# Kernel optimization log

Measured on AMD Instinct MI355X. Metric: run time of the kernel, lower is better.

Reference implementation:

```python
import jax, jax.numpy as jnp
import numpy as np

KSIZE = 3
SCALE = 2


def setup_inputs() -> dict:
    key = jax.random.key(0)
    k1, k2, k3, k4 = jax.random.split(key, 4)
    B, C, H, W = 8, 3, 512, 512
    h, w = H // SCALE, W // SCALE
    return {
        "images": jax.random.uniform(k1, (B, C, H, W), jnp.float32),
        "kernels": jax.random.uniform(k2, (B, KSIZE ** 2, h, w), jnp.float32),
        "offsets_x": jax.random.uniform(k3, (B, KSIZE ** 2, h, w), jnp.float32),
        "offsets_y": jax.random.uniform(k4, (B, KSIZE ** 2, h, w), jnp.float32),
    }


def _softround(x, alpha=1.0):
    two_pi = 2.0 * jnp.pi
    return x - alpha * (jnp.sin(two_pi * x) / two_pi)


def _batch_bli(im, x, y):
    # im: [B, H, W, 3] channel-last; x, y: [B, N] float coords
    B, N = x.shape
    x0 = jnp.floor(x).astype(jnp.int32)
    x1 = x0 + 1
    y0 = jnp.floor(y).astype(jnp.int32)
    y1 = y0 + 1
    # original clamps x by im.shape[2] and y by im.shape[1] (square images)
    x0 = jnp.clip(x0, 0, im.shape[2] - 1)
    x1 = jnp.clip(x1, 0, im.shape[2] - 1)
    y0 = jnp.clip(y0, 0, im.shape[1] - 1)
    y1 = jnp.clip(y1, 0, im.shape[1] - 1)
    bidx = jnp.arange(B)[:, None]
    # vectorized gather of the four corners; flatten like torch.cat of [3]-vectors
    Ia = im[bidx, x0, y0].reshape(-1)  # [B*N*3]
    Ib = im[bidx, x0, y1].reshape(-1)
    Ic = im[bidx, x1, y0].reshape(-1)
    Id = im[bidx, x1, y1].reshape(-1)
    scale_w = (1.0 / ((x1 - x0) * (y1 - y0))).reshape(-1)  # [B*N]
    # faithful to the original's (scrambling) reshape semantics
    m1 = jnp.concatenate([x1 - x, x - x0], axis=1).astype(jnp.float32)  # [B, 2N]
    m1 = jnp.tile(m1.reshape(B * N, 1, 1, 2), (1, 2, 1, 1))             # [BN,2,1,2]
    m2 = jnp.stack([Ib, Ia, Id, Ic], axis=1).reshape(B * N, 2, 2, 3)    # [BN,2,2,3]
    m3 = jnp.concatenate([y1 - y, y - y0], axis=1).astype(jnp.float32)
    m3 = m3.reshape(B * N, 1, 2, 1)                                     # [BN,1,2,1]
    t = jnp.matmul(m1, m2).transpose(0, 3, 2, 1)  # [BN,3,1,2]
    out = jnp.matmul(t, m3).reshape(B * N, 3)     # [BN,3]
    return scale_w[:, None] * out


def reference(images, kernels, offsets_x, offsets_y):
    B = images.shape[0]
    h, w = images.shape[2] // SCALE, images.shape[3] // SCALE
    kernels = kernels.transpose(0, 2, 3, 1)      # [B,h,w,9]
    ox = offsets_x.transpose(0, 2, 3, 1)         # [B,h,w,9]
    oy = offsets_y.transpose(0, 2, 3, 1)
    u = jnp.arange(h, dtype=jnp.float32) + 0.5 * SCALE - 0.5
    kx = jnp.repeat(jnp.arange(KSIZE), KSIZE).astype(jnp.float32)  # 0,0,0,1,1,1,2,2,2
    ky = jnp.tile(jnp.arange(KSIZE), KSIZE).astype(jnp.float32)    # 0,1,2,0,1,2,0,1,2
    # original broadcasts u.reshape(h,1) over the w axis (requires h == w)
    coords_x = ox + KSIZE / 2 + kx + u[:, None]
    coords_y = oy + KSIZE / 2 + ky + u[:, None]
    im = images.transpose(0, 2, 3, 1)  # [B,H,W,3]
    pix = _batch_bli(im, coords_x.reshape(B, -1), coords_y.reshape(B, -1))
    pix_hr = pix.reshape(B, h, w, KSIZE ** 2, 3)
    out = jnp.sum(kernels[..., None] * pix_hr, axis=-2)  # [B,h,w,3]
    return _softround(out * 255.0)
```

## Files before the change

kernel.cpp:

```cpp
#include <hip/hip_runtime.h>
#include <math.h>

#define BATCH 8
#define HI 512
#define WI 512
#define HO 256
#define WO 256
#define PLANE (HI*WI)
#define OPIX (HO*WO)
#define LROWS 68
#define LCOLS 10
#define LQ 11

__global__ __launch_bounds__(256) void downsampler_kernel(
    const float* __restrict__ images,
    const float* __restrict__ kernels,
    const float* __restrict__ offx,
    const float* __restrict__ offy,
    float* __restrict__ out)
{
    __shared__ float4 simg[LROWS * LQ];

    const int blk  = blockIdx.x;
    const int b    = blk >> 8;
    const int ihx  = (blk >> 2) & 63;
    const int w0   = (blk & 3) << 6;
    const int tid  = threadIdx.x;
    const int lane = tid & 63;
    const int iw   = w0 + lane;
    const int ih   = (ihx << 2) + (tid >> 6);

    const float* offxb = offx    + (size_t)b * 9 * OPIX;
    const float* offyb = offy    + (size_t)b * 9 * OPIX;
    const float* kernb = kernels + (size_t)b * 9 * OPIX;

    const int pl   = ih * WO + iw;
    const int pix2 = pl & (OPIX / 2 - 1);

    float  ox_[9], oy_[9], kv_[9];
    float2 sx_[9], sy_[9];
    #pragma unroll
    for (int k = 0; k < 9; ++k) {
        ox_[k] = offxb[k * OPIX + pl];
        oy_[k] = offyb[k * OPIX + pl];
        kv_[k] = kernb[k * OPIX + pl];
        sx_[k] = ((const float2*)(offxb + k * OPIX))[pix2];
        sy_[k] = ((const float2*)(offyb + k * OPIX))[pix2];
    }

    {
        const float* imb = images + (size_t)b * 3 * PLANE;
        #pragma unroll
        for (int ii = 0; ii < 3; ++ii) {
            const int i = tid + ii * 256;
            if (i < LROWS * LCOLS) {
                const int row = i / LCOLS;
                const int col = i - row * LCOLS;
                const int r = w0 + 2 + row;
                int c = r - 4 + col;
                c = c < 0 ? 0 : c;
                const float* src = imb + r * WI + c;
                simg[row * LQ + col] =
                    make_float4(src[0], src[PLANE], src[2 * PLANE], 0.0f);
            }
        }
    }
    __builtin_amdgcn_sched_barrier(0);
    __syncthreads();

    const bool flip = (ih < 128);
    const float uu_own = (float)iw + 0.5f;
    const float uu_s0  = (float)((2 * iw) & 255) + 0.5f;
    const float uu_s1  = uu_s0 + 1.0f;

    float acc0 = 0.f, acc1 = 0.f, acc2 = 0.f;

    #pragma unroll
    for (int k = 0; k < 9; ++k) {
        const float kxf = (float)(k / 3);
        const float kyf = (float)(k - 3 * (k / 3));
        const float cx = ((ox_[k] + 1.5f) + kxf) + uu_own;
        const float cy = ((oy_[k] + 1.5f) + kyf) + uu_own;
        const int x0 = (int)floorf(cx);
        const int y0 = (int)floorf(cy);
        const int rowrel = x0 - 2 - w0;
        const int colq   = y0 - x0 + 4;
        const float4* qa = &simg[rowrel * LQ + (colq - 1)];
        const float4 Ia = qa[1];
        const float4 Ib = qa[2];
        const float4 Ic = qa[LQ];
        const float4 Id = qa[LQ + 1];

        const int ta = 2 * k, tb = 2 * k + 1;
        const int sel_a = (ta >= 9) ? 1 : 0;
        const int sel_b = (tb >= 9) ? 1 : 0;
        const int ks_a = ta - 9 * sel_a;
        const int ks_b = tb - 9 * sel_b;
        const float uu_a = sel_a ? uu_s1 : uu_s0;
        const float uu_b = sel_b ? uu_s1 : uu_s0;
        const float oxa  = sel_a ? sx_[ks_a].y : sx_[ks_a].x;
        const float oya  = sel_a ? sy_[ks_a].y : sy_[ks_a].x;
        const float oxb2 = sel_b ? sx_[ks_b].y : sx_[ks_b].x;
        const float oyb2 = sel_b ? sy_[ks_b].y : sy_[ks_b].x;
        const float kxa = (float)(ks_a / 3), kya = (float)(ks_a - 3 * (ks_a / 3));
        const float kxb = (float)(ks_b / 3), kyb = (float)(ks_b - 3 * (ks_b / 3));

        const float cxa = ((oxa + 1.5f) + kxa) + uu_a;
        const float cya = ((oya + 1.5f) + kya) + uu_a;
        const float cxb = ((oxb2 + 1.5f) + kxb) + uu_b;
        const float cyb = ((oyb2 + 1.5f) + kyb) + uu_b;
        const float fxa = cxa - floorf(cxa);
        const float fya = cya - floorf(cya);
        const float fxb = cxb - floorf(cxb);
        const float fyb = cyb - floorf(cyb);
        const float w0w = flip ? (1.0f - fxa) : fxa;
        const float w1w = flip ? (1.0f - fxb) : fxb;
        const float v0w = flip ? (1.0f - fya) : fya;
        const float v1w = flip ? (1.0f - fyb) : fyb;

        const float w0v0 = w0w * v0w, w1v0 = w1w * v0w;
        const float w0v1 = w0w * v1w, w1v1 = w1w * v1w;

        const float p0 = w0v0 * Ib.x + w1v0 * Ic.x + w0v1 * Id.y + w1v1 * Ia.z;
        const float p1 = w0v0 * Ia.x + w1v0 * Ib.y + w0v1 * Ic.y + w1v1 * Id.z;
        const float p2 = w0v0 * Id.x + w1v0 * Ia.y + w0v1 * Ib.z + w1v1 * Ic.z;

        acc0 += kv_[k] * p0;
        acc1 += kv_[k] * p1;
        acc2 += kv_[k] * p2;
    }

    const float TWO_PI_INV = 0.15915494309189533577f;
    const size_t obase = ((size_t)b * OPIX + (size_t)pl) * 3;
    const float z0 = acc0 * 255.0f;
    const float z1 = acc1 * 255.0f;
    const float z2 = acc2 * 255.0f;
    const float r0s = z0 - rintf(z0);
    const float r1s = z1 - rintf(z1);
    const float r2s = z2 - rintf(z2);
    out[obase + 0] = z0 - __builtin_amdgcn_sinf(r0s) * TWO_PI_INV;
    out[obase + 1] = z1 - __builtin_amdgcn_sinf(r1s) * TWO_PI_INV;
    out[obase + 2] = z2 - __builtin_amdgcn_sinf(r2s) * TWO_PI_INV;
}

extern "C" void kernel_launch(void* const* d_in, const int* in_sizes, int n_in,
                              void* d_out, int out_size, void* d_ws, size_t ws_size,
                              hipStream_t stream) {
    const float* images  = (const float*)d_in[0];
    const float* kernels = (const float*)d_in[1];
    const float* offx    = (const float*)d_in[2];
    const float* offy    = (const float*)d_in[3];
    float* out = (float*)d_out;

    dim3 grid(BATCH * 64 * 4);
    dim3 block(256);
    hipLaunchKernelGGL(downsampler_kernel, grid, block, 0, stream,
                       images, kernels, offx, offy, out);
}
```

Measured before the change: 113.0 us.

## Process paired half-plane pixels per thread to share scrambled offset loads

Each thread now computes two output pixels, pl and pl+HALF. Because of the reference's reshape scrambling, both pixels use the same scrambled float2 offset pair for their weights, so those loads and the fractional-weight math are shared and the flip branch is removed. The grid is halved, launch bounds request 4 blocks, and the LDS byte offsets are computed before the barrier to overlap with the shared-memory fill. The cost is higher register pressure and fewer blocks in flight.

```diff
diff --git a/kernel.cpp b/kernel.cpp
--- a/kernel.cpp
+++ b/kernel.cpp
@@ -8,11 +8,12 @@
 #define WO 256
 #define PLANE (HI*WI)
 #define OPIX (HO*WO)
+#define HALF (OPIX/2)
 #define LROWS 68
 #define LCOLS 10
 #define LQ 11
 
-__global__ __launch_bounds__(256) void downsampler_kernel(
+__global__ __launch_bounds__(256, 4) void downsampler_kernel(
     const float* __restrict__ images,
     const float* __restrict__ kernels,
     const float* __restrict__ offx,
@@ -22,30 +23,37 @@
     __shared__ float4 simg[LROWS * LQ];
 
     const int blk  = blockIdx.x;
-    const int b    = blk >> 8;
-    const int ihx  = (blk >> 2) & 63;
+    const int b    = blk >> 7;
+    const int ihx  = (blk >> 2) & 31;
     const int w0   = (blk & 3) << 6;
     const int tid  = threadIdx.x;
     const int lane = tid & 63;
     const int iw   = w0 + lane;
-    const int ih   = (ihx << 2) + (tid >> 6);
+    const int ihA  = (ihx << 2) + (tid >> 6);
+    const int plA  = ihA * WO + iw;
+    const int plB  = plA + HALF;
 
     const float* offxb = offx    + (size_t)b * 9 * OPIX;
     const float* offyb = offy    + (size_t)b * 9 * OPIX;
     const float* kernb = kernels + (size_t)b * 9 * OPIX;
 
-    const int pl   = ih * WO + iw;
-    const int pix2 = pl & (OPIX / 2 - 1);
-
-    float  ox_[9], oy_[9], kv_[9];
+    float oxA[9], oyA[9], oxB[9], oyB[9];
+    #pragma unroll
+    for (int k = 0; k < 9; ++k) {
+        oxA[k] = offxb[k * OPIX + plA];
+        oyA[k] = offyb[k * OPIX + plA];
+        oxB[k] = offxb[k * OPIX + plB];
+        oyB[k] = offyb[k * OPIX + plB];
+    }
+
     float2 sx_[9], sy_[9];
-    #pragma unroll
-    for (int k = 0; k < 9; ++k) {
-        ox_[k] = offxb[k * OPIX + pl];
-        oy_[k] = offyb[k * OPIX + pl];
-        kv_[k] = kernb[k * OPIX + pl];
-        sx_[k] = ((const float2*)(offxb + k * OPIX))[pix2];
-        sy_[k] = ((const float2*)(offyb + k * OPIX))[pix2];
+    float  kvA[9], kvB[9];
+    #pragma unroll
+    for (int k = 0; k < 9; ++k) {
+        sx_[k] = ((const float2*)(offxb + k * OPIX))[plA];
+        sy_[k] = ((const float2*)(offyb + k * OPIX))[plA];
+        kvA[k] = kernb[k * OPIX + plA];
+        kvB[k] = kernb[k * OPIX + plB];
     }
 
     {
@@ -65,32 +73,40 @@
             }
         }
     }
+
+    const float uu_own = (float)iw + 0.5f;
+    int offA9[9], offB9[9];
+    #pragma unroll
+    for (int k = 0; k < 9; ++k) {
+        const float kxf = (float)(k / 3);
+        const float kyf = (float)(k - 3 * (k / 3));
+        {
+            const float cx = ((oxA[k] + 1.5f) + kxf) + uu_own;
+            const float cy = ((oyA[k] + 1.5f) + kyf) + uu_own;
+            const int x0 = (int)floorf(cx);
+            const int y0 = (int)floorf(cy);
+            offA9[k] = (((x0 - 2 - w0) * LQ) + (y0 - x0 + 3)) << 4;
+        }
+        {
+            const float cx = ((oxB[k] + 1.5f) + kxf) + uu_own;
+            const float cy = ((oyB[k] + 1.5f) + kyf) + uu_own;
+            const int x0 = (int)floorf(cx);
+            const int y0 = (int)floorf(cy);
+            offB9[k] = (((x0 - 2 - w0) * LQ) + (y0 - x0 + 3)) << 4;
+        }
+    }
     __builtin_amdgcn_sched_barrier(0);
     __syncthreads();
 
-    const bool flip = (ih < 128);
-    const float uu_own = (float)iw + 0.5f;
-    const float uu_s0  = (float)((2 * iw) & 255) + 0.5f;
-    const float uu_s1  = uu_s0 + 1.0f;
-
-    float acc0 = 0.f, acc1 = 0.f, acc2 = 0.f;
-
-    #pragma unroll
-    for (int k = 0; k < 9; ++k) {
-        const float kxf = (float)(k / 3);
-        const float kyf = (float)(k - 3 * (k / 3));
-        const float cx = ((ox_[k] + 1.5f) + kxf) + uu_own;
-        const float cy = ((oy_[k] + 1.5f) + kyf) + uu_own;
-        const int x0 = (int)floorf(cx);
-        const int y0 = (int)floorf(cy);
-        const int rowrel = x0 - 2 - w0;
-        const int colq   = y0 - x0 + 4;
-        const float4* qa = &simg[rowrel * LQ + (colq - 1)];
-        const float4 Ia = qa[1];
-        const float4 Ib = qa[2];
-        const float4 Ic = qa[LQ];
-        const float4 Id = qa[LQ + 1];
-
+    const float uu_s0 = (float)((2 * iw) & 255) + 0.5f;
+    const float uu_s1 = uu_s0 + 1.0f;
+
+    float aA0 = 0.f, aA1 = 0.f, aA2 = 0.f;
+    float aB0 = 0.f, aB1 = 0.f, aB2 = 0.f;
+    const char* sbase = (const char*)simg;
+
+    #pragma unroll
+    for (int k = 0; k < 9; ++k) {
         const int ta = 2 * k, tb = 2 * k + 1;
         const int sel_a = (ta >= 9) ? 1 : 0;
         const int sel_b = (tb >= 9) ? 1 : 0;
@@ -113,34 +129,65 @@
         const float fya = cya - floorf(cya);
         const float fxb = cxb - floorf(cxb);
         const float fyb = cyb - floorf(cyb);
-        const float w0w = flip ? (1.0f - fxa) : fxa;
-        const float w1w = flip ? (1.0f - fxb) : fxb;
-        const float v0w = flip ? (1.0f - fya) : fya;
-        const float v1w = flip ? (1.0f - fyb) : fyb;
-
-        const float w0v0 = w0w * v0w, w1v0 = w1w * v0w;
-        const float w0v1 = w0w * v1w, w1v1 = w1w * v1w;
-
-        const float p0 = w0v0 * Ib.x + w1v0 * Ic.x + w0v1 * Id.y + w1v1 * Ia.z;
-        const float p1 = w0v0 * Ia.x + w1v0 * Ib.y + w0v1 * Ic.y + w1v1 * Id.z;
-        const float p2 = w0v0 * Id.x + w1v0 * Ia.y + w0v1 * Ib.z + w1v1 * Ic.z;
-
-        acc0 += kv_[k] * p0;
-        acc1 += kv_[k] * p1;
-        acc2 += kv_[k] * p2;
+
+        const float w0A = 1.0f - fxa, w1A = 1.0f - fxb;
+        const float v0A = 1.0f - fya, v1A = 1.0f - fyb;
+        const float A00 = w0A * v0A, A10 = w1A * v0A, A01 = w0A * v1A, A11 = w1A * v1A;
+        const float B00 = fxa * fya, B10 = fxb * fya, B01 = fxa * fyb, B11 = fxb * fyb;
+
+        {
+            const float4* q = (const float4*)(sbase + offA9[k]);
+            const float4 Ia = q[1];
+            const float4 Ib = q[2];
+            const float4 Ic = q[LQ];
+            const float4 Id = q[LQ + 1];
+            const float p0 = A00 * Ib.x + A10 * Ic.x + A01 * Id.y + A11 * Ia.z;
+            const float p1 = A00 * Ia.x + A10 * Ib.y + A01 * Ic.y + A11 * Id.z;
+            const float p2 = A00 * Id.x + A10 * Ia.y + A01 * Ib.z + A11 * Ic.z;
+            aA0 += kvA[k] * p0;
+            aA1 += kvA[k] * p1;
+            aA2 += kvA[k] * p2;
+        }
+        {
+            const float4* q = (const float4*)(sbase + offB9[k]);
+            const float4 Ia = q[1];
+            const float4 Ib = q[2];
+            const float4 Ic = q[LQ];
+            const float4 Id = q[LQ + 1];
+            const float p0 = B00 * Ib.x + B10 * Ic.x + B01 * Id.y + B11 * Ia.z;
+            const float p1 = B00 * Ia.x + B10 * Ib.y + B01 * Ic.y + B11 * Id.z;
+            const float p2 = B00 * Id.x + B10 * Ia.y + B01 * Ib.z + B11 * Ic.z;
+            aB0 += kvB[k] * p0;
+            aB1 += kvB[k] * p1;
+            aB2 += kvB[k] * p2;
+        }
     }
 
     const float TWO_PI_INV = 0.15915494309189533577f;
-    const size_t obase = ((size_t)b * OPIX + (size_t)pl) * 3;
-    const float z0 = acc0 * 255.0f;
-    const float z1 = acc1 * 255.0f;
-    const float z2 = acc2 * 255.0f;
-    const float r0s = z0 - rintf(z0);
-    const float r1s = z1 - rintf(z1);
-    const float r2s = z2 - rintf(z2);
-    out[obase + 0] = z0 - __builtin_amdgcn_sinf(r0s) * TWO_PI_INV;
-    out[obase + 1] = z1 - __builtin_amdgcn_sinf(r1s) * TWO_PI_INV;
-    out[obase + 2] = z2 - __builtin_amdgcn_sinf(r2s) * TWO_PI_INV;
+    {
+        const size_t obase = ((size_t)b * OPIX + (size_t)plA) * 3;
+        const float z0 = aA0 * 255.0f;
+        const float z1 = aA1 * 255.0f;
+        const float z2 = aA2 * 255.0f;
+        const float r0s = z0 - rintf(z0);
+        const float r1s = z1 - rintf(z1);
+        const float r2s = z2 - rintf(z2);
+        out[obase + 0] = z0 - __builtin_amdgcn_sinf(r0s) * TWO_PI_INV;
+        out[obase + 1] = z1 - __builtin_amdgcn_sinf(r1s) * TWO_PI_INV;
+        out[obase + 2] = z2 - __builtin_amdgcn_sinf(r2s) * TWO_PI_INV;
+    }
+    {
+        const size_t obase = ((size_t)b * OPIX + (size_t)plB) * 3;
+        const float z0 = aB0 * 255.0f;
+        const float z1 = aB1 * 255.0f;
+        const float z2 = aB2 * 255.0f;
+        const float r0s = z0 - rintf(z0);
+        const float r1s = z1 - rintf(z1);
+        const float r2s = z2 - rintf(z2);
+        out[obase + 0] = z0 - __builtin_amdgcn_sinf(r0s) * TWO_PI_INV;
+        out[obase + 1] = z1 - __builtin_amdgcn_sinf(r1s) * TWO_PI_INV;
+        out[obase + 2] = z2 - __builtin_amdgcn_sinf(r2s) * TWO_PI_INV;
+    }
 }
 
 extern "C" void kernel_launch(void* const* d_in, const int* in_sizes, int n_in,
@@ -152,7 +199,7 @@
     const float* offy    = (const float*)d_in[3];
     float* out = (float*)d_out;
 
-    dim3 grid(BATCH * 64 * 4);
+    dim3 grid(BATCH * 32 * 4);
     dim3 block(256);
     hipLaunchKernelGGL(downsampler_kernel, grid, block, 0, stream,
                        images, kernels, offx, offy, out);
```

Measured after the change: 114.5 us. About the same (+1.4%).
